# Kernel optimization log

Hardware: AMD Instinct MI355X
Metric: run time of the kernel (lower is better)

Reference implementation:

```python
import jax, jax.numpy as jnp
import numpy as np

N_NODES = 100000
N_EDGES = 1600000
F_IN, HIDDEN, N_CLASS = 64, 48, 40


def setup_inputs() -> dict:
    key = jax.random.key(0)
    ks = jax.random.split(key, 9)
    def glorot(k, fi, fo):
        s = (6.0 / (fi + fo)) ** 0.5
        return jax.random.uniform(k, (fi, fo), jnp.float32, -s, s)
    return {
        "x": jax.random.normal(ks[0], (N_NODES, F_IN), jnp.float32),
        "edge_index": jax.random.randint(ks[1], (2, N_EDGES), 0, N_NODES, jnp.int64),
        "edge_weight": jax.random.uniform(ks[2], (N_EDGES,), jnp.float32),
        "W1": glorot(ks[3], F_IN, HIDDEN),   # ARMAConv init_weight (K=1)
        "V1": glorot(ks[4], F_IN, HIDDEN),   # ARMAConv root_weight
        "b1": jnp.zeros((HIDDEN,), jnp.float32),
        "W2": glorot(ks[5], HIDDEN, N_CLASS),
        "V2": glorot(ks[6], HIDDEN, N_CLASS),
        "b2": jnp.zeros((N_CLASS,), jnp.float32),
    }


def _arma_conv(x, W, V, b, src, dst, norm, num_nodes):
    # out = ReLU( A_norm @ (x @ W) + x @ V + b )   (num_stacks=1, num_layers=1)
    h = x @ W                                   # [N, F_out]
    msg = h[src] * norm[:, None]                # gather + scale  [E, F_out]
    agg = jax.ops.segment_sum(msg, dst, num_segments=num_nodes)  # scatter-add
    return jax.nn.relu(agg + x @ V + b)


def reference(x, edge_index, edge_weight, W1, V1, b1, W2, V2, b2):
    num_nodes = x.shape[0]
    src, dst = edge_index[0], edge_index[1]
    # gcn_norm, add_self_loops=False: D^{-1/2} A D^{-1/2}
    deg = jax.ops.segment_sum(edge_weight, dst, num_segments=num_nodes)
    dinv = jnp.where(deg > 0, jax.lax.rsqrt(jnp.where(deg > 0, deg, 1.0)), 0.0)
    norm = dinv[src] * edge_weight * dinv[dst]
    # eval mode: input dropout is identity
    h = _arma_conv(x, W1, V1, b1, src, dst, norm, num_nodes)
    h = _arma_conv(h, W2, V2, b2, src, dst, norm, num_nodes)
    return jax.nn.log_softmax(h, axis=-1)
```

## Files before the change

### kernel.cpp

```cpp
#include <hip/hip_runtime.h>
#include <math.h>


constexpr int F_IN = 64;
constexpr int HIDDEN = 48;
constexpr int N_CLASS = 40;
constexpr int CHUNK = 4096;
constexpr int EPT = CHUNK / 256;
constexpr int BIN_SHIFT = 9;
constexpr int BIN_CAP = 9216;
constexpr int CSR_CAP = 12288;

typedef __attribute__((ext_vector_type(8))) short bf16x8;
typedef __attribute__((ext_vector_type(4))) float f32x4;

__device__ __forceinline__ short bfr(float f) {
    unsigned u = __float_as_uint(f);
    return (short)((u + 0x7fffu + ((u >> 16) & 1u)) >> 16);
}
__device__ __forceinline__ unsigned pack_bf2(float a, float b) {
    unsigned ua = __float_as_uint(a), ub = __float_as_uint(b);
    ua = (ua + 0x7fffu + ((ua >> 16) & 1u)) >> 16;
    ub = (ub + 0x7fffu + ((ub >> 16) & 1u)) >> 16;
    return ua | (ub << 16);
}
__device__ __forceinline__ float2 unpack_bf2(unsigned u) {
    return make_float2(__uint_as_float(u << 16), __uint_as_float(u & 0xffff0000u));
}
__device__ __forceinline__ bf16x8 cvt8(float4 f0, float4 f1) {
    bf16x8 r;
    r[0] = bfr(f0.x); r[1] = bfr(f0.y); r[2] = bfr(f0.z); r[3] = bfr(f0.w);
    r[4] = bfr(f1.x); r[5] = bfr(f1.y); r[6] = bfr(f1.z); r[7] = bfr(f1.w);
    return r;
}

__global__ void init_cursor(int* __restrict__ binCursor) {
    binCursor[threadIdx.x] = (int)threadIdx.x * BIN_CAP;
}

__global__ __launch_bounds__(256) void gemm1_binscatter(
    const float* __restrict__ X, const float* __restrict__ W,
    const float* __restrict__ V, const float* __restrict__ b,
    unsigned* __restrict__ XWp, unsigned* __restrict__ AGGp, int N,
    const int* __restrict__ src, const int* __restrict__ dst,
    const float* __restrict__ w, int* __restrict__ binCursor,
    int2* __restrict__ binned, int E, int nSc) {
    __shared__ char smem[36864];
    int tid = threadIdx.x;

    if ((int)blockIdx.x < nSc) {
        int* hist = (int*)smem;
        hist[tid] = 0;
        __syncthreads();
        long long e0 = (long long)blockIdx.x * CHUNK;
        int M = (int)min((long long)CHUNK, (long long)E - e0);
        int dv[EPT], sv[EPT], wv[EPT];
#pragma unroll
        for (int q = 0; q < EPT; ++q) {
            int i = tid + q * 256;
            if (i < M) {
                dv[q] = dst[e0 + i];
                sv[q] = src[e0 + i];
                wv[q] = __float_as_int(w[e0 + i]);
                atomicAdd(&hist[dv[q] >> BIN_SHIFT], 1);
            }
        }
        __syncthreads();
        int h = hist[tid];
        int base = h ? atomicAdd(&binCursor[tid], h) : 0;
        __syncthreads();
        hist[tid] = base;
        __syncthreads();
#pragma unroll
        for (int q = 0; q < EPT; ++q) {
            int i = tid + q * 256;
            if (i < M) {
                int d = dv[q];
                int p = atomicAdd(&hist[d >> BIN_SHIFT], 1);
                binned[p] = make_int2(((d & 511) << 17) | sv[q], wv[q]);
            }
        }
        return;
    }

    short* sWT = (short*)smem;
    float* ep = (float*)(smem + 12288);
    for (int i = tid; i < 96 * 64; i += 256) {
        int c = i >> 6, k = i & 63;
        float v = (c < 48) ? W[k * 48 + c] : V[k * 48 + (c - 48)];
        sWT[i] = bfr(v);
    }
    __syncthreads();

    int lane = tid & 63, wvq = tid >> 6;
    int m = lane & 15, quad = lane >> 4;
    int nb0 = ((int)blockIdx.x - nSc) * 64;
    int n = nb0 + wvq * 16 + m;

    bf16x8 a0, a1;
    if (n < N) {
        const float4* xr = (const float4*)(X + (size_t)n * 64 + quad * 8);
        a0 = cvt8(xr[0], xr[1]);
        const float4* xr2 = (const float4*)(X + (size_t)n * 64 + 32 + quad * 8);
        a1 = cvt8(xr2[0], xr2[1]);
    } else {
        for (int j = 0; j < 8; ++j) { a0[j] = 0; a1[j] = 0; }
    }

    f32x4 acc[6];
#pragma unroll
    for (int ct = 0; ct < 6; ++ct) acc[ct] = (f32x4){0.f, 0.f, 0.f, 0.f};
#pragma unroll
    for (int ct = 0; ct < 6; ++ct) {
        bf16x8 b0 = *(const bf16x8*)(sWT + (ct * 16 + m) * 64 + quad * 8);
        bf16x8 b1 = *(const bf16x8*)(sWT + (ct * 16 + m) * 64 + 32 + quad * 8);
        acc[ct] = __builtin_amdgcn_mfma_f32_16x16x32_bf16(a0, b0, acc[ct], 0, 0, 0);
        acc[ct] = __builtin_amdgcn_mfma_f32_16x16x32_bf16(a1, b1, acc[ct], 0, 0, 0);
    }
#pragma unroll
    for (int ct = 0; ct < 6; ++ct)
#pragma unroll
        for (int r = 0; r < 4; ++r)
            ep[(wvq * 16 + quad * 4 + r) * 96 + ct * 16 + m] = acc[ct][r];
    __syncthreads();
    for (int i = tid; i < 64 * 24; i += 256) {
        int r = i / 24, c2 = i - r * 24;
        int node = nb0 + r;
        if (node >= N) continue;
        float w0 = ep[r * 96 + 2 * c2], w1 = ep[r * 96 + 2 * c2 + 1];
        XWp[node * 24 + c2] = pack_bf2(w0, w1);
        float v0 = ep[r * 96 + 48 + 2 * c2], v1 = ep[r * 96 + 48 + 2 * c2 + 1];
        float2 bb = ((const float2*)b)[c2];
        AGGp[node * 24 + c2] = pack_bf2(v0 + bb.x, v1 + bb.y);
    }
}

__global__ __launch_bounds__(512) void build_csr(const int2* __restrict__ binned,
                                                 const int* __restrict__ binCursor,
                                                 int* __restrict__ rowBeg,
                                                 int* __restrict__ rowEnd,
                                                 float* __restrict__ dinv,
                                                 unsigned* __restrict__ csr,
                                                 unsigned* __restrict__ XW1p, int N) {
    __shared__ int sx[CSR_CAP];
    __shared__ int sw[CSR_CAP];
    __shared__ int cntL[512];
    __shared__ float degL[512];
    __shared__ int scanL[512];
    int b = blockIdx.x, tid = threadIdx.x;
    int e0 = b * BIN_CAP;
    int M = min(binCursor[b] - e0, BIN_CAP);
    cntL[tid] = 0;
    degL[tid] = 0.f;
    __syncthreads();
    for (int i = tid; i < M; i += 512) {
        int2 p = binned[e0 + i];
        sx[i] = p.x;
        sw[i] = p.y;
        int dl = ((unsigned)p.x) >> 17;
        atomicAdd(&cntL[dl], 1);
        atomicAdd(&degL[dl], __int_as_float(p.y));
    }
    __syncthreads();
    int v = cntL[tid];
    scanL[tid] = v;
    __syncthreads();
#pragma unroll
    for (int o = 1; o < 512; o <<= 1) {
        int u = (tid >= o) ? scanL[tid - o] : 0;
        __syncthreads();
        scanL[tid] += u;
        __syncthreads();
    }
    int excl = scanL[tid] - v;
    int node = (b << BIN_SHIFT) + tid;
    float dg = degL[tid];
    float dv = dg > 0.f ? rsqrtf(dg) : 0.f;
    if (node < N) {
        rowBeg[node] = e0 + excl;
        rowEnd[node] = e0 + excl + v;
        dinv[node] = dv;
    }
    cntL[tid] = e0 + excl;
    degL[tid] = dv;
    __syncthreads();
    for (int i = tid; i < M; i += 512) {
        int px = sx[i], pw = sw[i];
        int dl = ((unsigned)px) >> 17;
        int pos = atomicAdd(&cntL[dl], 1);
        float wn = __int_as_float(pw) * degL[dl];
        unsigned uw = __float_as_uint(wn);
        uw = (uw + 0x7fffu + ((uw >> 16) & 1u)) >> 16;
        csr[pos] = ((unsigned)(px & 0x1FFFF) << 15) | uw;
    }
    int nb0 = b << BIN_SHIFT;
    for (int i = tid; i < 512 * 24; i += 512) {
        int nl = i / 24, c = i - nl * 24;
        int nn = nb0 + nl;
        if (nn >= N) break;
        float dvn = degL[nl];
        float2 u = unpack_bf2(XW1p[nn * 24 + c]);
        XW1p[nn * 24 + c] = pack_bf2(u.x * dvn, u.y * dvn);
    }
}

template <int W>
__device__ __forceinline__ void edge1w(const unsigned* __restrict__ XWp,
                                       unsigned p, int c, float4& s0, float4& s1) {
    uint4 u = *(const uint4*)(XWp + (p >> 15) * W + c);
    float nr = __uint_as_float((p & 0x7FFFu) << 16);
    float2 x0 = unpack_bf2(u.x), x1 = unpack_bf2(u.y);
    float2 x2 = unpack_bf2(u.z), x3 = unpack_bf2(u.w);
    s0.x = fmaf(x0.x, nr, s0.x); s0.y = fmaf(x0.y, nr, s0.y);
    s0.z = fmaf(x1.x, nr, s0.z); s0.w = fmaf(x1.y, nr, s0.w);
    s1.x = fmaf(x2.x, nr, s1.x); s1.y = fmaf(x2.y, nr, s1.y);
    s1.z = fmaf(x3.x, nr, s1.z); s1.w = fmaf(x3.y, nr, s1.w);
}

template <int W>
__device__ __forceinline__ void edge4w(const unsigned* __restrict__ XWp, uint4 p4,
                                       int c, float4& s0, float4& s1) {
    uint4 u0 = *(const uint4*)(XWp + (p4.x >> 15) * W + c);
    uint4 u1 = *(const uint4*)(XWp + (p4.y >> 15) * W + c);
    uint4 u2 = *(const uint4*)(XWp + (p4.z >> 15) * W + c);
    uint4 u3 = *(const uint4*)(XWp + (p4.w >> 15) * W + c);
    float n0 = __uint_as_float((p4.x & 0x7FFFu) << 16);
    float n1 = __uint_as_float((p4.y & 0x7FFFu) << 16);
    float n2 = __uint_as_float((p4.z & 0x7FFFu) << 16);
    float n3 = __uint_as_float((p4.w & 0x7FFFu) << 16);
    {
        float2 a0 = unpack_bf2(u0.x), a1 = unpack_bf2(u0.y);
        float2 a2 = unpack_bf2(u0.z), a3 = unpack_bf2(u0.w);
        s0.x = fmaf(a0.x, n0, s0.x); s0.y = fmaf(a0.y, n0, s0.y);
        s0.z = fmaf(a1.x, n0, s0.z); s0.w = fmaf(a1.y, n0, s0.w);
        s1.x = fmaf(a2.x, n0, s1.x); s1.y = fmaf(a2.y, n0, s1.y);
        s1.z = fmaf(a3.x, n0, s1.z); s1.w = fmaf(a3.y, n0, s1.w);
    }
    {
        float2 a0 = unpack_bf2(u1.x), a1 = unpack_bf2(u1.y);
        float2 a2 = unpack_bf2(u1.z), a3 = unpack_bf2(u1.w);
        s0.x = fmaf(a0.x, n1, s0.x); s0.y = fmaf(a0.y, n1, s0.y);
        s0.z = fmaf(a1.x, n1, s0.z); s0.w = fmaf(a1.y, n1, s0.w);
        s1.x = fmaf(a2.x, n1, s1.x); s1.y = fmaf(a2.y, n1, s1.y);
        s1.z = fmaf(a3.x, n1, s1.z); s1.w = fmaf(a3.y, n1, s1.w);
    }
    {
        float2 a0 = unpack_bf2(u2.x), a1 = unpack_bf2(u2.y);
        float2 a2 = unpack_bf2(u2.z), a3 = unpack_bf2(u2.w);
        s0.x = fmaf(a0.x, n2, s0.x); s0.y = fmaf(a0.y, n2, s0.y);
        s0.z = fmaf(a1.x, n2, s0.z); s0.w = fmaf(a1.y, n2, s0.w);
        s1.x = fmaf(a2.x, n2, s1.x); s1.y = fmaf(a2.y, n2, s1.y);
        s1.z = fmaf(a3.x, n2, s1.z); s1.w = fmaf(a3.y, n2, s1.w);
    }
    {
        float2 a0 = unpack_bf2(u3.x), a1 = unpack_bf2(u3.y);
        float2 a2 = unpack_bf2(u3.z), a3 = unpack_bf2(u3.w);
        s0.x = fmaf(a0.x, n3, s0.x); s0.y = fmaf(a0.y, n3, s0.y);
        s0.z = fmaf(a1.x, n3, s0.z); s0.w = fmaf(a1.y, n3, s0.w);
        s1.x = fmaf(a2.x, n3, s1.x); s1.y = fmaf(a2.y, n3, s1.y);
        s1.z = fmaf(a3.x, n3, s1.z); s1.w = fmaf(a3.y, n3, s1.w);
    }
}

template <int W>
__device__ __forceinline__ void row_accum4(const unsigned* __restrict__ XWp,
                                           const unsigned* __restrict__ csr,
                                           int j, int end, int c,
                                           float4& s0, float4& s1) {
    while (j < end && (j & 3)) {
        edge1w<W>(XWp, csr[j++], c, s0, s1);
    }
    int nch = (end - j) >> 2;
    if (nch > 0) {
        uint4 p4 = *(const uint4*)(csr + j);
        for (int k = 1; k < nch; ++k) {
            uint4 p4n = *(const uint4*)(csr + j + (k << 2));
            edge4w<W>(XWp, p4, c, s0, s1);
            p4 = p4n;
        }
        edge4w<W>(XWp, p4, c, s0, s1);
        j += nch << 2;
    }
    for (; j < end; ++j) {
        edge1w<W>(XWp, csr[j], c, s0, s1);
    }
}

__global__ __launch_bounds__(384) void pull_agg(const unsigned* __restrict__ XWp,
                                                const unsigned* __restrict__ csr,
                                                const int* __restrict__ rowBeg,
                                                const int* __restrict__ rowEnd,
                                                const unsigned* __restrict__ AGG1p,
                                                unsigned* __restrict__ H1p, int N) {
    int t = blockIdx.x * blockDim.x + threadIdx.x;
    int n = t / 6, c1 = t - n * 6;
    if (n >= N) return;
    int c = 4 * c1;
    uint4 a = *(const uint4*)(AGG1p + n * 24 + c);
    float2 f0 = unpack_bf2(a.x), f1 = unpack_bf2(a.y);
    float2 f2 = unpack_bf2(a.z), f3 = unpack_bf2(a.w);
    float4 s0 = make_float4(f0.x, f0.y, f1.x, f1.y);
    float4 s1 = make_float4(f2.x, f2.y, f3.x, f3.y);
    row_accum4<24>(XWp, csr, rowBeg[n], rowEnd[n], c, s0, s1);
    uint4 o;
    o.x = pack_bf2(fmaxf(s0.x, 0.f), fmaxf(s0.y, 0.f));
    o.y = pack_bf2(fmaxf(s0.z, 0.f), fmaxf(s0.w, 0.f));
    o.z = pack_bf2(fmaxf(s1.x, 0.f), fmaxf(s1.y, 0.f));
    o.w = pack_bf2(fmaxf(s1.z, 0.f), fmaxf(s1.w, 0.f));
    *(uint4*)(H1p + n * 24 + c) = o;
}

__global__ __launch_bounds__(256) void gemm2_kernel(
    const short* __restrict__ H1, const float* __restrict__ W,
    const float* __restrict__ V, const float* __restrict__ b,
    const float* __restrict__ dinv, unsigned* __restrict__ XWp,
    unsigned* __restrict__ AGGp, int N) {
    __shared__ char smem[30720];
    short* sWT = (short*)smem;
    float* ep = (float*)(smem + 10240);
    int tid = threadIdx.x;
    for (int i = tid; i < 80 * 64; i += 256) {
        int c = i >> 6, k = i & 63;
        float v = 0.f;
        if (k < 48) v = (c < 40) ? W[k * 40 + c] : V[k * 40 + (c - 40)];
        sWT[i] = bfr(v);
    }
    __syncthreads();

    int lane = tid & 63, wv = tid >> 6;
    int m = lane & 15, quad = lane >> 4;
    int nb0 = (int)blockIdx.x * 64;
    int n = nb0 + wv * 16 + m;

    bf16x8 a0, a1;
    if (n < N) {
        a0 = *(const bf16x8*)(H1 + (size_t)n * 48 + quad * 8);
        if (quad < 2) {
            a1 = *(const bf16x8*)(H1 + (size_t)n * 48 + 32 + quad * 8);
        } else {
            for (int j = 0; j < 8; ++j) a1[j] = 0;
        }
    } else {
        for (int j = 0; j < 8; ++j) { a0[j] = 0; a1[j] = 0; }
    }

    f32x4 acc[5];
#pragma unroll
    for (int ct = 0; ct < 5; ++ct) acc[ct] = (f32x4){0.f, 0.f, 0.f, 0.f};
#pragma unroll
    for (int ct = 0; ct < 5; ++ct) {
        bf16x8 b0 = *(const bf16x8*)(sWT + (ct * 16 + m) * 64 + quad * 8);
        bf16x8 b1 = *(const bf16x8*)(sWT + (ct * 16 + m) * 64 + 32 + quad * 8);
        acc[ct] = __builtin_amdgcn_mfma_f32_16x16x32_bf16(a0, b0, acc[ct], 0, 0, 0);
        acc[ct] = __builtin_amdgcn_mfma_f32_16x16x32_bf16(a1, b1, acc[ct], 0, 0, 0);
    }
#pragma unroll
    for (int ct = 0; ct < 5; ++ct)
#pragma unroll
        for (int r = 0; r < 4; ++r)
            ep[(wv * 16 + quad * 4 + r) * 80 + ct * 16 + m] = acc[ct][r];
    __syncthreads();
    for (int i = tid; i < 64 * 20; i += 256) {
        int r = i / 20, c2 = i - r * 20;
        int node = nb0 + r;
        if (node >= N) continue;
        float dv = dinv[node];
        float w0 = ep[r * 80 + 2 * c2], w1 = ep[r * 80 + 2 * c2 + 1];
        XWp[node * 20 + c2] = pack_bf2(w0 * dv, w1 * dv);
        float v0 = ep[r * 80 + 40 + 2 * c2], v1 = ep[r * 80 + 40 + 2 * c2 + 1];
        float2 bb = ((const float2*)b)[c2];
        AGGp[node * 20 + c2] = pack_bf2(v0 + bb.x, v1 + bb.y);
    }
}

__global__ __launch_bounds__(320) void pull_ls(const unsigned* __restrict__ XWp,
                                               const unsigned* __restrict__ csr,
                                               const int* __restrict__ rowBeg,
                                               const int* __restrict__ rowEnd,
                                               const unsigned* __restrict__ AGG2p,
                                               float* __restrict__ out, int N) {
    __shared__ float4 sbuf[64 * 10];
    __shared__ float sl[64];
    int tid = threadIdx.x;
    int nl = tid / 5, c1 = tid - nl * 5;
    int n = blockIdx.x * 64 + nl;
    int c = 4 * c1;
    float4 s0 = make_float4(0.f, 0.f, 0.f, 0.f);
    float4 s1 = make_float4(0.f, 0.f, 0.f, 0.f);
    if (n < N) {
        uint4 a = *(const uint4*)(AGG2p + n * 20 + c);
        float2 f0 = unpack_bf2(a.x), f1 = unpack_bf2(a.y);
        float2 f2 = unpack_bf2(a.z), f3 = unpack_bf2(a.w);
        s0 = make_float4(f0.x, f0.y, f1.x, f1.y);
        s1 = make_float4(f2.x, f2.y, f3.x, f3.y);
        row_accum4<20>(XWp, csr, rowBeg[n], rowEnd[n], c, s0, s1);
    }
    sbuf[(nl * 5 + c1) * 2] = s0;
    sbuf[(nl * 5 + c1) * 2 + 1] = s1;
    __syncthreads();
    if (tid < 64) {
        float m = 0.f;
        for (int k = 0; k < 10; ++k) {
            float4 v = sbuf[tid * 10 + k];
            m = fmaxf(m, fmaxf(fmaxf(v.x, v.y), fmaxf(v.z, v.w)));
        }
        float sum = 0.f;
        for (int k = 0; k < 10; ++k) {
            float4 v = sbuf[tid * 10 + k];
            sum += expf(fmaxf(v.x, 0.f) - m) + expf(fmaxf(v.y, 0.f) - m) +
                   expf(fmaxf(v.z, 0.f) - m) + expf(fmaxf(v.w, 0.f) - m);
        }
        sl[tid] = m + logf(sum);
    }
    __syncthreads();
    if (n < N) {
        float l = sl[nl];
        float4* op = (float4*)(out + (size_t)n * 40 + 8 * c1);
        op[0] = make_float4(fmaxf(s0.x, 0.f) - l, fmaxf(s0.y, 0.f) - l,
                            fmaxf(s0.z, 0.f) - l, fmaxf(s0.w, 0.f) - l);
        op[1] = make_float4(fmaxf(s1.x, 0.f) - l, fmaxf(s1.y, 0.f) - l,
                            fmaxf(s1.z, 0.f) - l, fmaxf(s1.w, 0.f) - l);
    }
}

extern "C" void kernel_launch(void* const* d_in, const int* in_sizes, int n_in,
                              void* d_out, int out_size, void* d_ws, size_t ws_size,
                              hipStream_t stream) {
    const float* x  = (const float*)d_in[0];
    const int*   ei = (const int*)d_in[1];
    const float* ew = (const float*)d_in[2];
    const float* W1 = (const float*)d_in[3];
    const float* V1 = (const float*)d_in[4];
    const float* b1 = (const float*)d_in[5];
    const float* W2 = (const float*)d_in[6];
    const float* V2 = (const float*)d_in[7];
    const float* b2 = (const float*)d_in[8];
    float* out = (float*)d_out;

    const int N = in_sizes[0] / F_IN;
    const int E = in_sizes[2];
    const int* src = ei;
    const int* dst = ei + E;

    char* ws = (char*)d_ws;
    size_t off = 0;
    auto carve = [&](size_t bytes) {
        void* p = ws + off;
        off = (off + bytes + 255) & ~size_t(255);
        return p;
    };
    int*      binCursor = (int*)carve(256 * 4);
    int*      rowBeg    = (int*)carve((size_t)N * 4);
    int*      rowEnd    = (int*)carve((size_t)N * 4);
    float*    dinv      = (float*)carve((size_t)N * 4);
    int2*     binned    = (int2*)carve((size_t)256 * BIN_CAP * 8);
    unsigned* csr       = (unsigned*)carve((size_t)256 * BIN_CAP * 4);
    unsigned* xW1p      = (unsigned*)carve((size_t)N * 24 * 4);
    unsigned* agg1p     = (unsigned*)carve((size_t)N * 24 * 4);
    unsigned* h1p       = (unsigned*)carve((size_t)N * 24 * 4);
    unsigned* xW2p      = (unsigned*)carve((size_t)N * 20 * 4);
    unsigned* agg2p     = (unsigned*)carve((size_t)N * 20 * 4);

    const int B = 256;
    auto cdiv = [](long long a, long long b) { return (int)((a + b - 1) / b); };
    const int nSc = cdiv(E, CHUNK);
    const int nBins = (N + (1 << BIN_SHIFT) - 1) >> BIN_SHIFT;
    const int nGemmBlocks = cdiv(N, 64);

    init_cursor<<<1, 256, 0, stream>>>(binCursor);
    gemm1_binscatter<<<nSc + nGemmBlocks, B, 0, stream>>>(
        x, W1, V1, b1, xW1p, agg1p, N, src, dst, ew, binCursor, binned, E, nSc);
    build_csr<<<nBins, 512, 0, stream>>>(binned, binCursor, rowBeg, rowEnd,
                                         dinv, csr, xW1p, N);

    pull_agg<<<cdiv((long long)N * 6, 384), 384, 0, stream>>>(xW1p, csr, rowBeg,
                                                              rowEnd, agg1p, h1p, N);

    gemm2_kernel<<<nGemmBlocks, B, 0, stream>>>((const short*)h1p, W2, V2, b2,
                                                dinv, xW2p, agg2p, N);

    pull_ls<<<cdiv(N, 64), 320, 0, stream>>>(xW2p, csr, rowBeg, rowEnd,
                                             agg2p, out, N);
}
```

Baseline: 254.9 us.

## Fuse layer-1 pull aggregation with layer-2 MFMA GEMM via shared memory

Merges the pull_agg kernel and gemm2_kernel into one kernel. Each 384-thread block aggregates 64 nodes into an LDS tile of H1, then runs the MFMA GEMM on that tile. This removes the H1 global round trip and one launch. In exchange, LDS use per block rises, the GEMM waits on the slowest row in its block, and only 256 of the 384 threads do the MFMA work.

```diff
diff --git a/kernel.cpp b/kernel.cpp
--- a/kernel.cpp
+++ b/kernel.cpp
@@ -286,90 +286,85 @@
     }
 }
 
-__global__ __launch_bounds__(384) void pull_agg(const unsigned* __restrict__ XWp,
-                                                const unsigned* __restrict__ csr,
-                                                const int* __restrict__ rowBeg,
-                                                const int* __restrict__ rowEnd,
-                                                const unsigned* __restrict__ AGG1p,
-                                                unsigned* __restrict__ H1p, int N) {
-    int t = blockIdx.x * blockDim.x + threadIdx.x;
-    int n = t / 6, c1 = t - n * 6;
-    if (n >= N) return;
-    int c = 4 * c1;
-    uint4 a = *(const uint4*)(AGG1p + n * 24 + c);
-    float2 f0 = unpack_bf2(a.x), f1 = unpack_bf2(a.y);
-    float2 f2 = unpack_bf2(a.z), f3 = unpack_bf2(a.w);
-    float4 s0 = make_float4(f0.x, f0.y, f1.x, f1.y);
-    float4 s1 = make_float4(f2.x, f2.y, f3.x, f3.y);
-    row_accum4<24>(XWp, csr, rowBeg[n], rowEnd[n], c, s0, s1);
-    uint4 o;
-    o.x = pack_bf2(fmaxf(s0.x, 0.f), fmaxf(s0.y, 0.f));
-    o.y = pack_bf2(fmaxf(s0.z, 0.f), fmaxf(s0.w, 0.f));
-    o.z = pack_bf2(fmaxf(s1.x, 0.f), fmaxf(s1.y, 0.f));
-    o.w = pack_bf2(fmaxf(s1.z, 0.f), fmaxf(s1.w, 0.f));
-    *(uint4*)(H1p + n * 24 + c) = o;
-}
-
-__global__ __launch_bounds__(256) void gemm2_kernel(
-    const short* __restrict__ H1, const float* __restrict__ W,
+__global__ __launch_bounds__(384) void pull_gemm2(
+    const unsigned* __restrict__ XWp, const unsigned* __restrict__ csr,
+    const int* __restrict__ rowBeg, const int* __restrict__ rowEnd,
+    const unsigned* __restrict__ AGG1p, const float* __restrict__ W,
     const float* __restrict__ V, const float* __restrict__ b,
-    const float* __restrict__ dinv, unsigned* __restrict__ XWp,
-    unsigned* __restrict__ AGGp, int N) {
-    __shared__ char smem[30720];
-    short* sWT = (short*)smem;
-    float* ep = (float*)(smem + 10240);
+    const float* __restrict__ dinv, unsigned* __restrict__ XW2p,
+    unsigned* __restrict__ AGG2p, int N) {
+    __shared__ short sWT[80 * 64];
+    __shared__ short h1s[64 * 48];
+    __shared__ float ep[64 * 80];
     int tid = threadIdx.x;
-    for (int i = tid; i < 80 * 64; i += 256) {
+    int nb0 = (int)blockIdx.x * 64;
+
+    for (int i = tid; i < 80 * 64; i += 384) {
         int c = i >> 6, k = i & 63;
         float v = 0.f;
         if (k < 48) v = (c < 40) ? W[k * 40 + c] : V[k * 40 + (c - 40)];
         sWT[i] = bfr(v);
     }
-    __syncthreads();
-
-    int lane = tid & 63, wv = tid >> 6;
-    int m = lane & 15, quad = lane >> 4;
-    int nb0 = (int)blockIdx.x * 64;
-    int n = nb0 + wv * 16 + m;
-
-    bf16x8 a0, a1;
+
+    int nl = tid / 6, c1 = tid - nl * 6;
+    int n = nb0 + nl;
+    int c = 4 * c1;
     if (n < N) {
-        a0 = *(const bf16x8*)(H1 + (size_t)n * 48 + quad * 8);
+        uint4 a = *(const uint4*)(AGG1p + n * 24 + c);
+        float2 f0 = unpack_bf2(a.x), f1 = unpack_bf2(a.y);
+        float2 f2 = unpack_bf2(a.z), f3 = unpack_bf2(a.w);
+        float4 s0 = make_float4(f0.x, f0.y, f1.x, f1.y);
+        float4 s1 = make_float4(f2.x, f2.y, f3.x, f3.y);
+        row_accum4<24>(XWp, csr, rowBeg[n], rowEnd[n], c, s0, s1);
+        uint4 o;
+        o.x = pack_bf2(fmaxf(s0.x, 0.f), fmaxf(s0.y, 0.f));
+        o.y = pack_bf2(fmaxf(s0.z, 0.f), fmaxf(s0.w, 0.f));
+        o.z = pack_bf2(fmaxf(s1.x, 0.f), fmaxf(s1.y, 0.f));
+        o.w = pack_bf2(fmaxf(s1.z, 0.f), fmaxf(s1.w, 0.f));
+        *(uint4*)(h1s + nl * 48 + 8 * c1) = o;
+    } else {
+        uint4 z = make_uint4(0, 0, 0, 0);
+        *(uint4*)(h1s + nl * 48 + 8 * c1) = z;
+    }
+    __syncthreads();
+
+    if (tid < 256) {
+        int lane = tid & 63, wv = tid >> 6;
+        int m = lane & 15, quad = lane >> 4;
+        bf16x8 a0 = *(const bf16x8*)(h1s + (wv * 16 + m) * 48 + quad * 8);
+        bf16x8 a1;
         if (quad < 2) {
-            a1 = *(const bf16x8*)(H1 + (size_t)n * 48 + 32 + quad * 8);
+            a1 = *(const bf16x8*)(h1s + (wv * 16 + m) * 48 + 32 + quad * 8);
         } else {
             for (int j = 0; j < 8; ++j) a1[j] = 0;
         }
-    } else {
-        for (int j = 0; j < 8; ++j) { a0[j] = 0; a1[j] = 0; }
-    }
-
-    f32x4 acc[5];
-#pragma unroll
-    for (int ct = 0; ct < 5; ++ct) acc[ct] = (f32x4){0.f, 0.f, 0.f, 0.f};
-#pragma unroll
-    for (int ct = 0; ct < 5; ++ct) {
-        bf16x8 b0 = *(const bf16x8*)(sWT + (ct * 16 + m) * 64 + quad * 8);
-        bf16x8 b1 = *(const bf16x8*)(sWT + (ct * 16 + m) * 64 + 32 + quad * 8);
-        acc[ct] = __builtin_amdgcn_mfma_f32_16x16x32_bf16(a0, b0, acc[ct], 0, 0, 0);
-        acc[ct] = __builtin_amdgcn_mfma_f32_16x16x32_bf16(a1, b1, acc[ct], 0, 0, 0);
-    }
-#pragma unroll
-    for (int ct = 0; ct < 5; ++ct)
-#pragma unroll
-        for (int r = 0; r < 4; ++r)
-            ep[(wv * 16 + quad * 4 + r) * 80 + ct * 16 + m] = acc[ct][r];
-    __syncthreads();
-    for (int i = tid; i < 64 * 20; i += 256) {
+        f32x4 acc[5];
+#pragma unroll
+        for (int ct = 0; ct < 5; ++ct) acc[ct] = (f32x4){0.f, 0.f, 0.f, 0.f};
+#pragma unroll
+        for (int ct = 0; ct < 5; ++ct) {
+            bf16x8 b0 = *(const bf16x8*)(sWT + (ct * 16 + m) * 64 + quad * 8);
+            bf16x8 b1 = *(const bf16x8*)(sWT + (ct * 16 + m) * 64 + 32 + quad * 8);
+            acc[ct] = __builtin_amdgcn_mfma_f32_16x16x32_bf16(a0, b0, acc[ct], 0, 0, 0);
+            acc[ct] = __builtin_amdgcn_mfma_f32_16x16x32_bf16(a1, b1, acc[ct], 0, 0, 0);
+        }
+#pragma unroll
+        for (int ct = 0; ct < 5; ++ct)
+#pragma unroll
+            for (int r = 0; r < 4; ++r)
+                ep[(wv * 16 + quad * 4 + r) * 80 + ct * 16 + m] = acc[ct][r];
+    }
+    __syncthreads();
+    for (int i = tid; i < 64 * 20; i += 384) {
         int r = i / 20, c2 = i - r * 20;
         int node = nb0 + r;
         if (node >= N) continue;
         float dv = dinv[node];
         float w0 = ep[r * 80 + 2 * c2], w1 = ep[r * 80 + 2 * c2 + 1];
-        XWp[node * 20 + c2] = pack_bf2(w0 * dv, w1 * dv);
+        XW2p[node * 20 + c2] = pack_bf2(w0 * dv, w1 * dv);
         float v0 = ep[r * 80 + 40 + 2 * c2], v1 = ep[r * 80 + 40 + 2 * c2 + 1];
         float2 bb = ((const float2*)b)[c2];
-        AGGp[node * 20 + c2] = pack_bf2(v0 + bb.x, v1 + bb.y);
+        AGG2p[node * 20 + c2] = pack_bf2(v0 + bb.x, v1 + bb.y);
     }
 }
 
@@ -457,7 +452,6 @@
     unsigned* csr       = (unsigned*)carve((size_t)256 * BIN_CAP * 4);
     unsigned* xW1p      = (unsigned*)carve((size_t)N * 24 * 4);
     unsigned* agg1p     = (unsigned*)carve((size_t)N * 24 * 4);
-    unsigned* h1p       = (unsigned*)carve((size_t)N * 24 * 4);
     unsigned* xW2p      = (unsigned*)carve((size_t)N * 20 * 4);
     unsigned* agg2p     = (unsigned*)carve((size_t)N * 20 * 4);
 
@@ -473,11 +467,9 @@
     build_csr<<<nBins, 512, 0, stream>>>(binned, binCursor, rowBeg, rowEnd,
                                          dinv, csr, xW1p, N);
 
-    pull_agg<<<cdiv((long long)N * 6, 384), 384, 0, stream>>>(xW1p, csr, rowBeg,
-                                                              rowEnd, agg1p, h1p, N);
-
-    gemm2_kernel<<<nGemmBlocks, B, 0, stream>>>((const short*)h1p, W2, V2, b2,
-                                                dinv, xW2p, agg2p, N);
+    pull_gemm2<<<nGemmBlocks, 384, 0, stream>>>(xW1p, csr, rowBeg, rowEnd,
+                                                agg1p, W2, V2, b2, dinv,
+                                                xW2p, agg2p, N);
 
     pull_ls<<<cdiv(N, 64), 320, 0, stream>>>(xW2p, csr, rowBeg, rowEnd,
                                              agg2p, out, N);
```

Result: no change. 253.1 us (-0.7%).
